# Kernel optimization log

Hardware: AMD Instinct MI355X
Metric: run time of the kernel (lower is better)

## Reference

```python
import jax, jax.numpy as jnp
import numpy as np

EMBED = 1024
HEADS = 16
HEAD_DIM = EMBED // HEADS


def setup_inputs() -> dict:
    key = jax.random.key(0)
    ks = jax.random.split(key, 8)
    N, L = 2, 2048
    s = 0.02
    return {
        "values": jax.random.normal(ks[0], (N, L, EMBED), jnp.float32),
        "keys": jax.random.normal(ks[1], (N, L, EMBED), jnp.float32),
        "queries": jax.random.normal(ks[2], (N, L, EMBED), jnp.float32),
        # per-head projection weights, SHARED across heads (nn.Linear(head_dim, head_dim))
        "Wv": jax.random.normal(ks[3], (HEAD_DIM, HEAD_DIM), jnp.float32) * s,
        "Wk": jax.random.normal(ks[4], (HEAD_DIM, HEAD_DIM), jnp.float32) * s,
        "Wq": jax.random.normal(ks[5], (HEAD_DIM, HEAD_DIM), jnp.float32) * s,
        "Wo": jax.random.normal(ks[6], (EMBED, EMBED), jnp.float32) * s,
        "bo": jax.random.normal(ks[7], (EMBED,), jnp.float32) * s,
    }


def reference(values, keys, queries, Wv, Wk, Wq, Wo, bo):
    N, Lq, _ = queries.shape
    Lk = keys.shape[1]
    Lv = values.shape[1]
    # split heads: (N, L, H, D)
    v = values.reshape(N, Lv, HEADS, HEAD_DIM)
    k = keys.reshape(N, Lk, HEADS, HEAD_DIM)
    q = queries.reshape(N, Lq, HEADS, HEAD_DIM)
    # per-head linear (weight shared across heads); nn.Linear computes x @ W.T
    v = jnp.einsum('nlhd,ed->nlhe', v, Wv)
    k = jnp.einsum('nlhd,ed->nlhe', k, Wk)
    q = jnp.einsum('nlhd,ed->nlhe', q, Wq)
    # scores (N, H, Lq, Lk); NOTE: scale uses sqrt(embed_size), as in the original
    scores = jnp.einsum('nqhd,nkhd->nhqk', q, k) / jnp.sqrt(jnp.float32(EMBED))
    attn = jax.nn.softmax(scores, axis=-1)
    out = jnp.einsum('nhql,nlhd->nqhd', attn, v).reshape(N, Lq, EMBED)
    out = out @ Wo.T + bo
    return out
```

## Files before the change

### kernel.cpp

```cpp
#include <hip/hip_runtime.h>
#include <hip/hip_bf16.h>

#define EMBED 1024
#define HEADS 16
#define HD 64
#define NB 2
#define LSEQ 2048

typedef __bf16 bf16x8 __attribute__((ext_vector_type(8)));
typedef float f32x4 __attribute__((ext_vector_type(4)));

static __device__ __forceinline__ __bf16 f2b(float x) {
    union { __hip_bfloat16 h; __bf16 b; } u;
    u.h = __float2bfloat16(x);
    return u.b;
}
static __device__ __forceinline__ bf16x8 cvt8(float4 a, float4 b) {
    bf16x8 r;
    r[0] = f2b(a.x); r[1] = f2b(a.y); r[2] = f2b(a.z); r[3] = f2b(a.w);
    r[4] = f2b(b.x); r[5] = f2b(b.y); r[6] = f2b(b.z); r[7] = f2b(b.w);
    return r;
}
static __device__ __forceinline__ unsigned short b2u(float x) {
    union { __hip_bfloat16 h; unsigned short u; } c;
    c.h = __float2bfloat16(x);
    return c.u;
}

#define GLD16(g, l) __builtin_amdgcn_global_load_lds( \
    (const __attribute__((address_space(1))) void*)(g), \
    (__attribute__((address_space(3))) void*)(l), 16, 0, 0)


__global__ __launch_bounds__(256) void proj_kernel(
    const float* __restrict__ vals,
    const float* __restrict__ keys,
    const float* __restrict__ quer,
    const float* __restrict__ Wv,
    const float* __restrict__ Wk,
    const float* __restrict__ Wq,
    const float* __restrict__ Wo,
    __hip_bfloat16* __restrict__ QF,
    __hip_bfloat16* __restrict__ KF,
    __hip_bfloat16* __restrict__ VF,
    __hip_bfloat16* __restrict__ Wob)
{
    if (blockIdx.x >= 1536) {
        int base = ((blockIdx.x - 1536) * 256 + threadIdx.x) * 16;
#pragma unroll
        for (int j = 0; j < 16; j += 4) {
            float4 w4 = *(const float4*)(Wo + base + j);
            __hip_bfloat16 o[4] = {
                __float2bfloat16(w4.x), __float2bfloat16(w4.y),
                __float2bfloat16(w4.z), __float2bfloat16(w4.w)};
            *(ushort4*)(Wob + base + j) = *(const ushort4*)o;
        }
        return;
    }

    int b      = blockIdx.x;
    int tensor = b % 3;
    int rem    = b / 3;
    int n      = rem >> 8;
    int lt     = (rem >> 3) & 31;
    int hp     = rem & 7;
    int t = threadIdx.x, w = t >> 6, lane = t & 63;
    int m16 = lane & 15, quad = lane >> 4;
    int l0 = lt * 64 + w * 16;

    const float* X = (tensor == 0) ? quer : (tensor == 1 ? keys : vals);
    const float* W = (tensor == 0) ? Wq   : (tensor == 1 ? Wk   : Wv);
    float scale = (tensor == 0) ? (1.44269504088896340736f / 32.0f) : 1.0f;

    const float* xb = X + ((size_t)n * LSEQ + l0 + m16) * EMBED + (hp * 2) * HD + quad * 8;
    bf16x8 xf[2][2];
#pragma unroll
    for (int hh = 0; hh < 2; ++hh)
#pragma unroll
        for (int kk = 0; kk < 2; ++kk) {
            const float* xp = xb + hh * HD + kk * 32;
            xf[hh][kk] = cvt8(*(const float4*)xp, *(const float4*)(xp + 4));
        }

    bf16x8 wf[4][2];
#pragma unroll
    for (int f = 0; f < 4; ++f)
#pragma unroll
        for (int kk = 0; kk < 2; ++kk) {
            const float* wp = W + (f * 16 + m16) * HD + kk * 32 + quad * 8;
            wf[f][kk] = cvt8(*(const float4*)wp, *(const float4*)(wp + 4));
        }

#pragma unroll
    for (int hh = 0; hh < 2; ++hh) {
        int h = hp * 2 + hh;
        size_t nhb = (size_t)(n * HEADS + h) * 131072;
        if (tensor != 2) {
            f32x4 acc[4] = {};
#pragma unroll
            for (int f = 0; f < 4; ++f) {
                acc[f] = __builtin_amdgcn_mfma_f32_16x16x32_bf16(wf[f][0], xf[hh][0], acc[f], 0, 0, 0);
                acc[f] = __builtin_amdgcn_mfma_f32_16x16x32_bf16(wf[f][1], xf[hh][1], acc[f], 0, 0, 0);
            }
            int key = l0 + m16;
#pragma unroll
            for (int f = 0; f < 4; ++f) {
                union { ushort4 u; unsigned short s[4]; } p;
#pragma unroll
                for (int r = 0; r < 4; ++r) p.s[r] = b2u(acc[f][r] * scale);
                int kk   = f >> 1;
                int qk2  = (f & 1) * 2 + (quad >> 1);
                int j4   = (quad & 1) * 4;
                __hip_bfloat16* dst;
                if (tensor == 0) {
                    dst = QF + nhb + (size_t)(l0 >> 4) * 1024 + kk * 512
                        + (qk2 * 16 + m16) * 8 + j4;
                } else {
                    dst = KF + nhb + (size_t)(key >> 5) * 2048
                        + ((key & 1) * 2 + kk) * 512
                        + (qk2 * 16 + ((key & 31) >> 1)) * 8 + j4;
                }
                *(ushort4*)dst = p.u;
            }
        } else {
            f32x4 acc[4] = {};
#pragma unroll
            for (int f = 0; f < 4; ++f) {
                acc[f] = __builtin_amdgcn_mfma_f32_16x16x32_bf16(xf[hh][0], wf[f][0], acc[f], 0, 0, 0);
                acc[f] = __builtin_amdgcn_mfma_f32_16x16x32_bf16(xf[hh][1], wf[f][1], acc[f], 0, 0, 0);
            }
            int keyq  = l0 + quad * 4;
            int c     = keyq >> 5;
            int quadv = (keyq & 31) >> 3;
            int j4    = (quad & 1) * 4;
#pragma unroll
            for (int f = 0; f < 4; ++f) {
                union { ushort4 u; unsigned short s[4]; } p;
#pragma unroll
                for (int r = 0; r < 4; ++r) p.s[r] = b2u(acc[f][r]);
                __hip_bfloat16* dst = VF + nhb + (size_t)c * 2048 + f * 512
                    + quadv * 128 + m16 * 8 + j4;
                *(ushort4*)dst = p.u;
            }
        }
    }
}

#define CHUNKS 32

#define LOADK(KFR, c_) do { \
    const __hip_bfloat16* kc_ = kp + (size_t)(c_) * 2048; \
    KFR[0][0] = *(const bf16x8*)(kc_); \
    KFR[0][1] = *(const bf16x8*)(kc_ + 512); \
    KFR[1][0] = *(const bf16x8*)(kc_ + 1024); \
    KFR[1][1] = *(const bf16x8*)(kc_ + 1536); \
} while (0)

#define LOADV(c_) do { \
    const __hip_bfloat16* vc_ = vp + (size_t)(c_) * 2048; \
    vf[0] = *(const bf16x8*)(vc_); \
    vf[1] = *(const bf16x8*)(vc_ + 512); \
    vf[2] = *(const bf16x8*)(vc_ + 1024); \
    vf[3] = *(const bf16x8*)(vc_ + 1536); \
} while (0)

#define SCOREX(KFR, PF) do { \
    f32x4 s_[2][2]; \
    __builtin_amdgcn_s_setprio(1); \
    _Pragma("unroll") \
    for (int tq_ = 0; tq_ < 2; ++tq_) { \
        _Pragma("unroll") \
        for (int t2_ = 0; t2_ < 2; ++t2_) { \
            f32x4 z_; \
            z_ = __builtin_amdgcn_mfma_f32_16x16x32_bf16(KFR[t2_][0], qf[tq_][0], zf, 0, 0, 0); \
            z_ = __builtin_amdgcn_mfma_f32_16x16x32_bf16(KFR[t2_][1], qf[tq_][1], z_, 0, 0, 0); \
            s_[tq_][t2_] = z_; \
        } \
    } \
    __builtin_amdgcn_s_setprio(0); \
    _Pragma("unroll") \
    for (int tq_ = 0; tq_ < 2; ++tq_) { \
        _Pragma("unroll") \
        for (int r_ = 0; r_ < 4; ++r_) { \
            PF[tq_][2 * r_]     = f2b(__builtin_amdgcn_exp2f(s_[tq_][0][r_])); \
            PF[tq_][2 * r_ + 1] = f2b(__builtin_amdgcn_exp2f(s_[tq_][1][r_])); \
        } \
    } \
} while (0)

#define PVX(PF) do { \
    __builtin_amdgcn_s_setprio(1); \
    _Pragma("unroll") \
    for (int f_ = 0; f_ < 4; ++f_) { \
        of[0][f_] = __builtin_amdgcn_mfma_f32_16x16x32_bf16(vf[f_], PF[0], of[0][f_], 0, 0, 0); \
        of[1][f_] = __builtin_amdgcn_mfma_f32_16x16x32_bf16(vf[f_], PF[1], of[1][f_], 0, 0, 0); \
    } \
    lsa[0] = __builtin_amdgcn_mfma_f32_16x16x32_bf16(onesf, PF[0], lsa[0], 0, 0, 0); \
    lsa[1] = __builtin_amdgcn_mfma_f32_16x16x32_bf16(onesf, PF[1], lsa[1], 0, 0, 0); \
    __builtin_amdgcn_s_setprio(0); \
} while (0)

__global__ __launch_bounds__(256) void attn_kernel(
    const __hip_bfloat16* __restrict__ QF,
    const __hip_bfloat16* __restrict__ KF,
    const __hip_bfloat16* __restrict__ VF,
    __hip_bfloat16* __restrict__ AO)
{
    __shared__ __align__(16) float Cb[5120];

    int i  = blockIdx.x;
    int x  = i & 7, r2 = i >> 3;
    int nh = x * 4 + (r2 >> 5);
    int qblk = r2 & 31;

    int t = threadIdx.x, w = t >> 6, lane = t & 63;
    int m16 = lane & 15, quad = lane >> 4;
    int qh = w & 1, kh = w >> 1;
    int q0 = qblk * 64 + qh * 32;
    size_t nhb = (size_t)nh * 131072;

    const __hip_bfloat16* qb = QF + nhb + (size_t)(q0 >> 4) * 1024 + lane * 8;
    bf16x8 qf[2][2];
#pragma unroll
    for (int tq = 0; tq < 2; ++tq)
#pragma unroll
        for (int kk = 0; kk < 2; ++kk)
            qf[tq][kk] = *(const bf16x8*)(qb + tq * 1024 + kk * 512);

    const __hip_bfloat16* kp = KF + nhb + (size_t)(kh * 32) * 2048 + lane * 8;
    const __hip_bfloat16* vp = VF + nhb + (size_t)(kh * 32) * 2048 + lane * 8;

    bf16x8 onesf;
#pragma unroll
    for (int j = 0; j < 8; ++j) onesf[j] = f2b(1.0f);
    const f32x4 zf = {};

    f32x4 of[2][4] = {};
    f32x4 lsa[2] = {};
    bf16x8 ka[2][2], kb[2][2], vf[4], pA[2], pB[2];

    LOADK(ka, 0);
    LOADK(kb, 1);
    SCOREX(ka, pA);
    LOADV(0);

#pragma unroll 1
    for (int tt = 0; tt < 15; ++tt) {
        int c = 2 * tt;
        LOADK(ka, c + 2);
        SCOREX(kb, pB);
        PVX(pA);
        LOADV(c + 1);
        LOADK(kb, c + 3);
        SCOREX(ka, pA);
        PVX(pB);
        LOADV(c + 2);
    }
    SCOREX(kb, pB);
    PVX(pA);
    LOADV(31);
    PVX(pB);

    __syncthreads();
    if (kh == 1) {
        int base = qh * 2560;
#pragma unroll
        for (int tq = 0; tq < 2; ++tq)
#pragma unroll
            for (int f = 0; f < 4; ++f)
                *(f32x4*)&Cb[base + (tq * 4 + f) * 256 + lane * 4] = of[tq][f];
#pragma unroll
        for (int tq = 0; tq < 2; ++tq)
            Cb[base + 2048 + tq * 64 + lane] = lsa[tq][0];
    }
    __syncthreads();
    if (kh == 0) {
        int base = qh * 2560;
#pragma unroll
        for (int tq = 0; tq < 2; ++tq)
#pragma unroll
            for (int f = 0; f < 4; ++f)
                of[tq][f] += *(const f32x4*)&Cb[base + (tq * 4 + f) * 256 + lane * 4];
        int n = nh >> 4, h = nh & 15;
#pragma unroll
        for (int tq = 0; tq < 2; ++tq) {
            float lt2 = lsa[tq][0] + Cb[base + 2048 + tq * 64 + lane];
            float rinv = 1.0f / lt2;
            int qrow = q0 + tq * 16 + m16;
#pragma unroll
            for (int f = 0; f < 4; ++f) {
                union { ushort4 u; unsigned short s[4]; } pk;
#pragma unroll
                for (int r = 0; r < 4; ++r) pk.s[r] = b2u(of[tq][f][r] * rinv);
                int col = h * HD + f * 16 + quad * 4;
                *(ushort4*)&AO[((size_t)n * LSEQ + qrow) * EMBED + col] = pk.u;
            }
        }
    }
}

__global__ __launch_bounds__(256) void outproj_kernel(
    const __hip_bfloat16* __restrict__ AO,
    const __hip_bfloat16* __restrict__ Wob,
    const float* __restrict__ bo,
    float* __restrict__ out)
{
    __shared__ __align__(16) __hip_bfloat16 As[2][2][64][32];
    __shared__ __align__(16) __hip_bfloat16 Bs[2][2][64][32];

    int b  = blockIdx.x;
    int wk = (b & 7) * 128 + (b >> 3);
    int mt = wk >> 4, nt = wk & 15;
    int m0 = mt * 64, n0 = nt * 64;
    int t = threadIdx.x, w = t >> 6, lane = t & 63;
    int m16 = lane & 15, quad = lane >> 4;

    int srow = lane >> 2;
    int scol = (lane & 3) * 8;

    const __hip_bfloat16* Ab = AO  + (size_t)m0 * EMBED;
    const __hip_bfloat16* Bb = Wob + (size_t)n0 * EMBED;

#define STAGE_OP(bb, k0_) do { \
    GLD16(Ab + (size_t)(w * 16 + srow) * EMBED + (k0_) +      scol, &As[bb][0][w * 16][0]); \
    GLD16(Ab + (size_t)(w * 16 + srow) * EMBED + (k0_) + 32 + scol, &As[bb][1][w * 16][0]); \
    GLD16(Bb + (size_t)(w * 16 + srow) * EMBED + (k0_) +      scol, &Bs[bb][0][w * 16][0]); \
    GLD16(Bb + (size_t)(w * 16 + srow) * EMBED + (k0_) + 32 + scol, &Bs[bb][1][w * 16][0]); \
} while (0)

    f32x4 acc[4] = {};
    STAGE_OP(0, 0);
    __syncthreads();

#pragma unroll 2
    for (int ks = 0; ks < 16; ++ks) {
        if (ks < 15) STAGE_OP((ks + 1) & 1, (ks + 1) * 64);
        int cur = ks & 1;
        bf16x8 af[2], bfr[2][4];
#pragma unroll
        for (int kk = 0; kk < 2; ++kk)
            af[kk] = *(const bf16x8*)&As[cur][kk][w * 16 + m16][quad * 8];
#pragma unroll
        for (int kk = 0; kk < 2; ++kk)
#pragma unroll
            for (int tb = 0; tb < 4; ++tb)
                bfr[kk][tb] = *(const bf16x8*)&Bs[cur][kk][tb * 16 + m16][quad * 8];
#pragma unroll
        for (int tb = 0; tb < 4; ++tb) {
            acc[tb] = __builtin_amdgcn_mfma_f32_16x16x32_bf16(af[0], bfr[0][tb], acc[tb], 0, 0, 0);
            acc[tb] = __builtin_amdgcn_mfma_f32_16x16x32_bf16(af[1], bfr[1][tb], acc[tb], 0, 0, 0);
        }
        __syncthreads();
    }

#pragma unroll
    for (int tb = 0; tb < 4; ++tb) {
        int col = n0 + tb * 16 + m16;
        float bias = bo[col];
#pragma unroll
        for (int r = 0; r < 4; ++r) {
            int row = m0 + w * 16 + quad * 4 + r;
            out[(size_t)row * EMBED + col] = acc[tb][r] + bias;
        }
    }
#undef STAGE_OP
}

extern "C" void kernel_launch(void* const* d_in, const int* in_sizes, int n_in,
                              void* d_out, int out_size, void* d_ws, size_t ws_size,
                              hipStream_t stream) {
    const float* vals = (const float*)d_in[0];
    const float* keys = (const float*)d_in[1];
    const float* quer = (const float*)d_in[2];
    const float* Wv   = (const float*)d_in[3];
    const float* Wk   = (const float*)d_in[4];
    const float* Wq   = (const float*)d_in[5];
    const float* Wo   = (const float*)d_in[6];
    const float* bo   = (const float*)d_in[7];
    float* out = (float*)d_out;

    __hip_bfloat16* ws = (__hip_bfloat16*)d_ws;
    const size_t PE = (size_t)NB * HEADS * LSEQ * HD;
    __hip_bfloat16* QF  = ws;
    __hip_bfloat16* KF  = ws + PE;
    __hip_bfloat16* VF  = ws + 2 * PE;
    __hip_bfloat16* AO  = ws + 3 * PE;
    __hip_bfloat16* Wob = ws + 4 * PE;

    proj_kernel<<<1536 + 256, 256, 0, stream>>>(
        vals, keys, quer, Wv, Wk, Wq, Wo, QF, KF, VF, Wob);
    attn_kernel<<<1024, 256, 0, stream>>>(QF, KF, VF, AO);
    outproj_kernel<<<1024, 256, 0, stream>>>(AO, Wob, bo, out);
}
```

Before: 169.1 us.

## Split attention key range four ways per block and double the grid

Each attention block now covers 32 query rows instead of 64, and its four waves each process a quarter of the keys (16 chunks) instead of two waves per query half splitting keys in half. The grid doubles to 2048 blocks and each wave's serial loop is half as long. The partial outputs and row sums are merged with a two-level reduction through shared memory. In exchange, every K/V chunk is read by twice as many blocks, and the merge adds one more shared-memory round and barrier.

After: 175.2 us. 1.04x slower.

```diff
diff --git a/kernel.cpp b/kernel.cpp
--- a/kernel.cpp
+++ b/kernel.cpp
@@ -146,7 +146,8 @@
     }
 }
 
-#define CHUNKS 32
+#define CHUNKS 16
+#define NIT ((CHUNKS - 2) / 2)
 
 #define LOADK(KFR, c_) do { \
     const __hip_bfloat16* kc_ = kp + (size_t)(c_) * 2048; \
@@ -206,17 +207,17 @@
     const __hip_bfloat16* __restrict__ VF,
     __hip_bfloat16* __restrict__ AO)
 {
-    __shared__ __align__(16) float Cb[5120];
+    __shared__ __align__(16) float Cb[4352];
 
     int i  = blockIdx.x;
     int x  = i & 7, r2 = i >> 3;
-    int nh = x * 4 + (r2 >> 5);
-    int qblk = r2 & 31;
+    int nh = x * 4 + (r2 >> 6);
+    int qblk = r2 & 63;
 
     int t = threadIdx.x, w = t >> 6, lane = t & 63;
     int m16 = lane & 15, quad = lane >> 4;
-    int qh = w & 1, kh = w >> 1;
-    int q0 = qblk * 64 + qh * 32;
+    int kh = w;
+    int q0 = qblk * 32;
     size_t nhb = (size_t)nh * 131072;
 
     const __hip_bfloat16* qb = QF + nhb + (size_t)(q0 >> 4) * 1024 + lane * 8;
@@ -227,8 +228,8 @@
         for (int kk = 0; kk < 2; ++kk)
             qf[tq][kk] = *(const bf16x8*)(qb + tq * 1024 + kk * 512);
 
-    const __hip_bfloat16* kp = KF + nhb + (size_t)(kh * 32) * 2048 + lane * 8;
-    const __hip_bfloat16* vp = VF + nhb + (size_t)(kh * 32) * 2048 + lane * 8;
+    const __hip_bfloat16* kp = KF + nhb + (size_t)(kh * CHUNKS) * 2048 + lane * 8;
+    const __hip_bfloat16* vp = VF + nhb + (size_t)(kh * CHUNKS) * 2048 + lane * 8;
 
     bf16x8 onesf;
 #pragma unroll
@@ -245,7 +246,7 @@
     LOADV(0);
 
 #pragma unroll 1
-    for (int tt = 0; tt < 15; ++tt) {
+    for (int tt = 0; tt < NIT; ++tt) {
         int c = 2 * tt;
         LOADK(ka, c + 2);
         SCOREX(kb, pB);
@@ -258,33 +259,53 @@
     }
     SCOREX(kb, pB);
     PVX(pA);
-    LOADV(31);
+    LOADV(CHUNKS - 1);
     PVX(pB);
 
+    __syncthreads();
+    if (kh >= 2) {
+        int base = (kh - 2) * 2176;
+#pragma unroll
+        for (int tq = 0; tq < 2; ++tq)
+#pragma unroll
+            for (int f = 0; f < 4; ++f)
+                *(f32x4*)&Cb[base + (tq * 4 + f) * 256 + lane * 4] = of[tq][f];
+#pragma unroll
+        for (int tq = 0; tq < 2; ++tq)
+            Cb[base + 2048 + tq * 64 + lane] = lsa[tq][0];
+    }
+    __syncthreads();
+    if (kh < 2) {
+        int base = kh * 2176;
+#pragma unroll
+        for (int tq = 0; tq < 2; ++tq)
+#pragma unroll
+            for (int f = 0; f < 4; ++f)
+                of[tq][f] += *(const f32x4*)&Cb[base + (tq * 4 + f) * 256 + lane * 4];
+#pragma unroll
+        for (int tq = 0; tq < 2; ++tq)
+            lsa[tq][0] += Cb[base + 2048 + tq * 64 + lane];
+    }
     __syncthreads();
     if (kh == 1) {
-        int base = qh * 2560;
 #pragma unroll
         for (int tq = 0; tq < 2; ++tq)
 #pragma unroll
             for (int f = 0; f < 4; ++f)
-                *(f32x4*)&Cb[base + (tq * 4 + f) * 256 + lane * 4] = of[tq][f];
-#pragma unroll
-        for (int tq = 0; tq < 2; ++tq)
-            Cb[base + 2048 + tq * 64 + lane] = lsa[tq][0];
+                *(f32x4*)&Cb[(tq * 4 + f) * 256 + lane * 4] = of[tq][f];
+#pragma unroll
+        for (int tq = 0; tq < 2; ++tq)
+            Cb[2048 + tq * 64 + lane] = lsa[tq][0];
     }
     __syncthreads();
     if (kh == 0) {
-        int base = qh * 2560;
-#pragma unroll
-        for (int tq = 0; tq < 2; ++tq)
+        int n = nh >> 4, h = nh & 15;
+#pragma unroll
+        for (int tq = 0; tq < 2; ++tq) {
 #pragma unroll
             for (int f = 0; f < 4; ++f)
-                of[tq][f] += *(const f32x4*)&Cb[base + (tq * 4 + f) * 256 + lane * 4];
-        int n = nh >> 4, h = nh & 15;
-#pragma unroll
-        for (int tq = 0; tq < 2; ++tq) {
-            float lt2 = lsa[tq][0] + Cb[base + 2048 + tq * 64 + lane];
+                of[tq][f] += *(const f32x4*)&Cb[(tq * 4 + f) * 256 + lane * 4];
+            float lt2 = lsa[tq][0] + Cb[2048 + tq * 64 + lane];
             float rinv = 1.0f / lt2;
             int qrow = q0 + tq * 16 + m16;
 #pragma unroll
@@ -389,6 +410,6 @@
 
     proj_kernel<<<1536 + 256, 256, 0, stream>>>(
         vals, keys, quer, Wv, Wk, Wq, Wo, QF, KF, VF, Wob);
-    attn_kernel<<<1024, 256, 0, stream>>>(QF, KF, VF, AO);
+    attn_kernel<<<2048, 256, 0, stream>>>(QF, KF, VF, AO);
     outproj_kernel<<<1024, 256, 0, stream>>>(AO, Wob, bo, out);
 }
```
